# Kernel optimization log

Measured on AMD Instinct MI355X. Metric: run time of the kernel, lower is better.

Reference implementation:

```python
import jax, jax.numpy as jnp
import numpy as np

U = 512   # units
D = 512   # decoder input feature dim
V = 46    # output vocab


def _lstm_cell(x_t, h, c, W, R, b):
    # Keras LSTMCell: gate order i, f, g(cell), o; sigmoid recurrent act, tanh act.
    z = x_t @ W + h @ R + b                      # [B, 4U]
    i, f, g, o = jnp.split(z, 4, axis=-1)
    i = jax.nn.sigmoid(i)
    f = jax.nn.sigmoid(f)
    g = jnp.tanh(g)
    o = jax.nn.sigmoid(o)
    c_new = f * c + i * g
    h_new = o * jnp.tanh(c_new)
    return h_new, c_new


def _lstm_seq(seq, W, R, b):
    # seq: [T, B, D]; zero initial state (Keras default). Returns (all h [T,B,U], last h [B,U]).
    B = seq.shape[1]
    u = R.shape[0]
    h0 = jnp.zeros((B, u), seq.dtype)
    c0 = jnp.zeros((B, u), seq.dtype)
    def step(carry, x_t):
        h, c = carry
        h, c = _lstm_cell(x_t, h, c, W, R, b)
        return (h, c), h
    (hT, _), hs = jax.lax.scan(step, (h0, c0), seq)
    return hs, hT


def setup_inputs() -> dict:
    key = jax.random.key(0)
    ks = jax.random.split(key, 10)
    def p(k, shape, scale=0.05):
        return jax.random.normal(k, shape, dtype=jnp.float32) * scale
    x = jax.random.normal(ks[0], (32, 512, U), dtype=jnp.float32)   # encoder outputs [B, S, U]
    y = jax.random.normal(ks[1], (32, 128, D), dtype=jnp.float32)   # decoder inputs  [B, T, D]
    return {
        "x": x, "y": y,
        "W_a": p(ks[2], (D, 4 * U)), "R_a": p(ks[3], (U, 4 * U)), "b_a": jnp.zeros((4 * U,), jnp.float32),
        "W1": p(ks[4], (U, 4 * U)), "R1": p(ks[5], (U, 4 * U)), "b1": jnp.zeros((4 * U,), jnp.float32),
        "W2": p(ks[6], (U, 4 * U)), "R2": p(ks[7], (U, 4 * U)), "b2": jnp.zeros((4 * U,), jnp.float32),
        "Wd": p(ks[8], (U, V)), "bd": jnp.zeros((V,), jnp.float32),
    }


def reference(x, y, W_a, R_a, b_a, W1, R1, b1, W2, R2, b2, Wd, bd):
    B = y.shape[0]
    yT = jnp.swapaxes(y, 0, 1)                          # [T, B, D]
    h0 = jnp.zeros((B, U), x.dtype)
    c0 = jnp.zeros((B, U), x.dtype)

    # AttentionLSTM: per-step LSTMCell + dot-product attention (Keras Attention,
    # unscaled, keys==values==x) + residual add of the context into both states.
    def step(carry, y_t):
        h, c = carry
        h, c = _lstm_cell(y_t, h, c, W_a, R_a, b_a)     # s = h  [B, U]
        scores = jnp.einsum('bu,bsu->bs', h, x)         # [B, S]
        ctx = jnp.einsum('bs,bsu->bu', jax.nn.softmax(scores, axis=-1), x)  # [B, U]
        return (h + ctx, c + ctx), ctx

    _, ctxs = jax.lax.scan(step, (h0, c0), yT)          # [T, B, U]

    # Stacked LSTMs: first returns full sequence, second returns last hidden state.
    hs1, _ = _lstm_seq(ctxs, W1, R1, b1)                # [T, B, U]
    _, hT = _lstm_seq(hs1, W2, R2, b2)                  # [B, U]

    logits = hT @ Wd + bd                               # [B, V]
    return jax.nn.softmax(logits, axis=-1)
```

## Files before the change

kernel.cpp:

```cpp
#include <hip/hip_runtime.h>
#include <math.h>


#define U_   512
#define S_   512
#define T_   128
#define B_   32
#define G4   2048
#define V_   46
#define NWG  256
#define FSTR 32

#define AT_LD(p)     __hip_atomic_load((p), __ATOMIC_RELAXED, __HIP_MEMORY_SCOPE_AGENT)
#define AT_ST(p, v)  __hip_atomic_store((p), (v), __ATOMIC_RELAXED, __HIP_MEMORY_SCOPE_AGENT)

__device__ __forceinline__ void group_bar(unsigned* gflags, unsigned* ggen,
                                          unsigned seq) {
  __syncthreads();
  const int tid = threadIdx.x;
  const int wgid = blockIdx.x & 31;
  if (wgid == 0) {
    if (tid < 64) {
      if (tid == 0) AT_ST(&gflags[0], seq);
      const int slot = tid & 31;
      while (!__all(AT_LD(&gflags[slot * FSTR]) >= seq))
        __builtin_amdgcn_s_sleep(1);
      if (tid == 0) AT_ST(ggen, seq);
    }
  } else {
    if (tid == 0) {
      AT_ST(&gflags[wgid * FSTR], seq);
      while (AT_LD(ggen) < seq) __builtin_amdgcn_s_sleep(1);
    }
  }
  __syncthreads();
}

__global__ __launch_bounds__(256) void gemm_k512(
    const float* __restrict__ A, const float* __restrict__ W,
    const float* __restrict__ b, float* __restrict__ Z) {
  const int tid = threadIdx.x;
  const int j = blockIdx.x * 1024 + tid * 4;
  const int i0 = blockIdx.y * 8;
  float4 bj = *(const float4*)(b + j);
  float4 acc[8];
#pragma unroll
  for (int r = 0; r < 8; ++r) acc[r] = bj;
  const float* Arow = A + (size_t)i0 * U_;
  for (int k = 0; k < U_; ++k) {
    float4 w = *(const float4*)(W + (size_t)k * G4 + j);
#pragma unroll
    for (int r = 0; r < 8; ++r) {
      float a = Arow[(size_t)r * U_ + k];
      acc[r].x = fmaf(a, w.x, acc[r].x);
      acc[r].y = fmaf(a, w.y, acc[r].y);
      acc[r].z = fmaf(a, w.z, acc[r].z);
      acc[r].w = fmaf(a, w.w, acc[r].w);
    }
  }
#pragma unroll
  for (int r = 0; r < 8; ++r)
    *(float4*)(Z + (size_t)(i0 + r) * G4 + j) = acc[r];
}

__global__ __launch_bounds__(256) void transpose_R(
    const float* __restrict__ R, float* __restrict__ RT) {
  __shared__ float tile[64][65];
  const int c0 = blockIdx.x * 64, k0 = blockIdx.y * 64;
  const int tc = threadIdx.x & 63, tr = threadIdx.x >> 6;
  for (int r = tr; r < 64; r += 4)
    tile[r][tc] = R[(size_t)(k0 + r) * G4 + c0 + tc];
  __syncthreads();
  for (int r = tr; r < 64; r += 4)
    RT[(size_t)(c0 + r) * 512 + k0 + tc] = tile[tc][r];
}

__global__ __launch_bounds__(512) void attn_coop(
    const float* __restrict__ x, const float* __restrict__ ZY,
    const float* __restrict__ RT, float* __restrict__ ctxs,
    float* hbuf, float* hnbuf, float* smax, float* ssumg,
    float* ctxpart, unsigned* flags, unsigned* gen) {
  extern __shared__ float dyn[];
  float* x_s  = dyn;
  float* h_st = dyn + 512 * 65;
  __shared__ float zp[4][64][2];
  __shared__ float hn_s[512];
  __shared__ float p_s[64];

  const int tid = threadIdx.x;
  const int bid = blockIdx.x;
  const int g    = bid >> 5;
  const int wgid = bid & 31;
  const int u0   = wgid * 16;
  const int kh  = tid & 1;
  const int b_l = (tid >> 1) & 3;
  const int col = tid >> 3;
  const int zcol = (col >> 4) * 512 + u0 + (col & 15);
  const int b_att = 4 * g + (wgid >> 3);
  const int sc = wgid & 7;
  unsigned* gflags = flags + g * 32 * FSTR;
  unsigned* ggen   = gen + g * FSTR;

  for (int idx = tid; idx < 64 * 512; idx += 512) {
    int sl = idx >> 9, u = idx & 511;
    x_s[u * 65 + sl] = x[((size_t)b_att * S_ + sc * 64 + sl) * U_ + u];
  }
  float c = 0.f, hn_reg = 0.f;
  unsigned seq = 0;
  __syncthreads();

  for (int t = 0; t < T_; ++t) {
    {
      const float* hb = hbuf + (t & 1) * 16384 + 4 * g * 512;
      for (int i = tid; i < 2048; i += 512)
        h_st[(i >> 9) * 516 + (i & 511)] = AT_LD(&hb[i]);
    }
    __syncthreads();
    {
      const float4* H4 = (const float4*)(h_st + b_l * 516 + kh * 256);
      const float4* R4 = (const float4*)(RT + (size_t)zcol * 512 + kh * 256);
      float acc = 0.f;
#pragma unroll 8
      for (int i = 0; i < 64; ++i) {
        float4 hv = H4[i];
        float4 rv = R4[i];
        acc = fmaf(hv.x, rv.x, acc); acc = fmaf(hv.y, rv.y, acc);
        acc = fmaf(hv.z, rv.z, acc); acc = fmaf(hv.w, rv.w, acc);
      }
      zp[b_l][col][kh] = acc;
    }
    __syncthreads();
    if (tid < 64) {
      const int bb = tid >> 4, uu = tid & 15;
      const int b = 4 * g + bb, u = u0 + uu;
      const float* zy = ZY + ((size_t)b * T_ + t) * G4 + u;
      float zi = zy[0]    + zp[bb][uu][0]      + zp[bb][uu][1];
      float zf = zy[512]  + zp[bb][16 + uu][0] + zp[bb][16 + uu][1];
      float zg = zy[1024] + zp[bb][32 + uu][0] + zp[bb][32 + uu][1];
      float zo = zy[1536] + zp[bb][48 + uu][0] + zp[bb][48 + uu][1];
      float ig = 1.f / (1.f + expf(-zi));
      float fg = 1.f / (1.f + expf(-zf));
      float gg = tanhf(zg);
      float og = 1.f / (1.f + expf(-zo));
      c = fg * c + ig * gg;
      hn_reg = og * tanhf(c);
      AT_ST(&hnbuf[b * 512 + u], hn_reg);
    }
    group_bar(gflags, ggen, ++seq);

    hn_s[tid] = AT_LD(&hnbuf[b_att * 512 + tid]);
    __syncthreads();
    {
      const int wv = tid >> 6, ln = tid & 63;
      for (int si = 0; si < 8; ++si) {
        const int sl = wv * 8 + si;
        float a = 0.f;
#pragma unroll
        for (int uu = ln; uu < 512; uu += 64)
          a = fmaf(hn_s[uu], x_s[uu * 65 + sl], a);
#pragma unroll
        for (int off = 32; off; off >>= 1) a += __shfl_down(a, off);
        if (ln == 0) p_s[sl] = a;
      }
    }
    __syncthreads();
    if (tid < 64) {
      float v = p_s[tid];
      float m = v;
#pragma unroll
      for (int off = 32; off; off >>= 1) m = fmaxf(m, __shfl_down(m, off));
      m = __shfl(m, 0);
      float ex = expf(v - m);
      p_s[tid] = ex;
      float sm = ex;
#pragma unroll
      for (int off = 32; off; off >>= 1) sm += __shfl_down(sm, off);
      if (tid == 0) {
        AT_ST(&smax[b_att * 8 + sc], m);
        AT_ST(&ssumg[b_att * 8 + sc], sm);
      }
    }
    __syncthreads();
    {
      float a = 0.f;
      const float* xr = x_s + tid * 65;
#pragma unroll 8
      for (int s = 0; s < 64; ++s) a = fmaf(p_s[s], xr[s], a);
      AT_ST(&ctxpart[((size_t)b_att * 8 + sc) * 512 + tid], a);
    }
    group_bar(gflags, ggen, ++seq);

    if (tid < 64) {
      const int bb = tid >> 4, uu = tid & 15;
      const int b = 4 * g + bb, u = u0 + uu;
      float lm[8], gm = -INFINITY;
#pragma unroll
      for (int j = 0; j < 8; ++j) {
        lm[j] = AT_LD(&smax[b * 8 + j]);
        gm = fmaxf(gm, lm[j]);
      }
      float stot = 0.f, cs = 0.f;
#pragma unroll
      for (int j = 0; j < 8; ++j) {
        float w = expf(lm[j] - gm);
        stot = fmaf(AT_LD(&ssumg[b * 8 + j]), w, stot);
        cs = fmaf(AT_LD(&ctxpart[((size_t)b * 8 + j) * 512 + u]), w, cs);
      }
      float ctxv = cs / stot;
      c += ctxv;
      float hcar = hn_reg + ctxv;
      AT_ST(&hbuf[((t + 1) & 1) * 16384 + b * 512 + u], hcar);
      ctxs[((size_t)b * T_ + t) * U_ + u] = ctxv;
    }
    group_bar(gflags, ggen, ++seq);
  }
}

__global__ __launch_bounds__(512) void lstm_coop(
    const float* __restrict__ Zin, const float* __restrict__ R,
    float* __restrict__ seq_out, float* __restrict__ last_out,
    float* hbuf, unsigned* flags, unsigned* gen) {
  extern __shared__ float dyn[];
  float* R_s  = dyn;
  float* h_st = dyn + 64 * 516;
  __shared__ float zp[4][64][2];
  const int tid = threadIdx.x;
  const int bid = blockIdx.x;
  const int g    = bid >> 5;
  const int wgid = bid & 31;
  const int u0   = wgid * 16;
  const int kh  = tid & 1;
  const int b_l = (tid >> 1) & 3;
  const int col = tid >> 3;
  unsigned* gflags = flags + g * 32 * FSTR;
  unsigned* ggen   = gen + g * FSTR;

  for (int idx = tid; idx < 64 * 512; idx += 512) {
    int cc = idx & 63, kk = idx >> 6;
    R_s[cc * 516 + kk] = R[(size_t)kk * G4 + (cc >> 4) * 512 + u0 + (cc & 15)];
  }
  float c = 0.f;
  unsigned seq = 0;
  __syncthreads();

  for (int t = 0; t < T_; ++t) {
    {
      const float* hb = hbuf + (t & 1) * 16384 + 4 * g * 512;
      for (int i = tid; i < 2048; i += 512)
        h_st[(i >> 9) * 516 + (i & 511)] = AT_LD(&hb[i]);
    }
    __syncthreads();
    {
      const float4* H4 = (const float4*)(h_st + b_l * 516 + kh * 256);
      const float4* R4 = (const float4*)(R_s + col * 516 + kh * 256);
      float acc = 0.f;
#pragma unroll 8
      for (int i = 0; i < 64; ++i) {
        float4 hv = H4[i];
        float4 rv = R4[i];
        acc = fmaf(hv.x, rv.x, acc); acc = fmaf(hv.y, rv.y, acc);
        acc = fmaf(hv.z, rv.z, acc); acc = fmaf(hv.w, rv.w, acc);
      }
      zp[b_l][col][kh] = acc;
    }
    __syncthreads();
    if (tid < 64) {
      const int bb = tid >> 4, uu = tid & 15;
      const int b = 4 * g + bb, u = u0 + uu;
      const float* zy = Zin + ((size_t)b * T_ + t) * G4 + u;
      float zi = zy[0]    + zp[bb][uu][0]      + zp[bb][uu][1];
      float zf = zy[512]  + zp[bb][16 + uu][0] + zp[bb][16 + uu][1];
      float zg = zy[1024] + zp[bb][32 + uu][0] + zp[bb][32 + uu][1];
      float zo = zy[1536] + zp[bb][48 + uu][0] + zp[bb][48 + uu][1];
      float ig = 1.f / (1.f + expf(-zi));
      float fg = 1.f / (1.f + expf(-zf));
      float gg = tanhf(zg);
      float og = 1.f / (1.f + expf(-zo));
      c = fg * c + ig * gg;
      float hv2 = og * tanhf(c);
      AT_ST(&hbuf[((t + 1) & 1) * 16384 + b * 512 + u], hv2);
      if (seq_out) seq_out[((size_t)b * T_ + t) * U_ + u] = hv2;
      if (last_out && t == T_ - 1) last_out[b * U_ + u] = hv2;
    }
    group_bar(gflags, ggen, ++seq);
  }
}

__global__ __launch_bounds__(64) void final_k(
    const float* __restrict__ hT, const float* __restrict__ Wd,
    const float* __restrict__ bd, float* __restrict__ out) {
  const int b = blockIdx.x;
  const int v = threadIdx.x;
  float acc = (v < V_) ? bd[v] : -INFINITY;
  if (v < V_) {
    for (int k = 0; k < U_; ++k)
      acc = fmaf(hT[(size_t)b * U_ + k], Wd[(size_t)k * V_ + v], acc);
  }
  float m = acc;
#pragma unroll
  for (int off = 32; off; off >>= 1) m = fmaxf(m, __shfl_down(m, off));
  m = __shfl(m, 0);
  float e = (v < V_) ? expf(acc - m) : 0.f;
  float s = e;
#pragma unroll
  for (int off = 32; off; off >>= 1) s += __shfl_down(s, off);
  s = __shfl(s, 0);
  if (v < V_) out[(size_t)b * V_ + v] = e / s;
}

extern "C" void kernel_launch(void* const* d_in, const int* in_sizes, int n_in,
                              void* d_out, int out_size, void* d_ws, size_t ws_size,
                              hipStream_t stream) {
  const float* x   = (const float*)d_in[0];
  const float* y   = (const float*)d_in[1];
  const float* W_a = (const float*)d_in[2];
  const float* R_a = (const float*)d_in[3];
  const float* b_a = (const float*)d_in[4];
  const float* W1  = (const float*)d_in[5];
  const float* R1  = (const float*)d_in[6];
  const float* b1  = (const float*)d_in[7];
  const float* W2  = (const float*)d_in[8];
  const float* R2  = (const float*)d_in[9];
  const float* b2  = (const float*)d_in[10];
  const float* Wd  = (const float*)d_in[11];
  const float* bd  = (const float*)d_in[12];
  float* out = (float*)d_out;

  float* ZBUF = (float*)d_ws;
  float* SEQ  = ZBUF + (size_t)8388608;
  float* RT   = SEQ + (size_t)2097152;
  float* HBUF = RT + (size_t)1048576;
  float* HN   = HBUF + 32768;
  float* SMAX = HN + 16384;
  float* SSUM = SMAX + 256;
  float* CTXP = SSUM + 256;
  float* HT   = CTXP + 131072;
  unsigned* BAR = (unsigned*)(HT + 16384);

  const int GRP = 32 * FSTR;
  const int REGION = 8 * GRP + 8 * FSTR;
  unsigned* FLG_A = BAR;                 unsigned* GEN_A = FLG_A + 8 * GRP;
  unsigned* FLG_1 = BAR + REGION;        unsigned* GEN_1 = FLG_1 + 8 * GRP;
  unsigned* FLG_2 = BAR + 2 * REGION;    unsigned* GEN_2 = FLG_2 + 8 * GRP;

  const int attn_lds = (512 * 65 + 4 * 516) * 4;
  const int lstm_lds = (64 * 516 + 4 * 516) * 4;
  hipFuncSetAttribute((const void*)attn_coop,
                      hipFuncAttributeMaxDynamicSharedMemorySize, attn_lds);
  hipFuncSetAttribute((const void*)lstm_coop,
                      hipFuncAttributeMaxDynamicSharedMemorySize, lstm_lds);

  dim3 ggrid(2, 512);
  hipMemsetAsync(BAR, 0, 3 * REGION * 4, stream);

  gemm_k512<<<ggrid, 256, 0, stream>>>(y, W_a, b_a, ZBUF);
  transpose_R<<<dim3(32, 8), 256, 0, stream>>>(R_a, RT);
  hipMemsetAsync(HBUF, 0, 32768 * 4, stream);
  attn_coop<<<NWG, 512, attn_lds, stream>>>(x, ZBUF, RT, SEQ, HBUF, HN,
                                            SMAX, SSUM, CTXP, FLG_A, GEN_A);
  gemm_k512<<<ggrid, 256, 0, stream>>>(SEQ, W1, b1, ZBUF);
  hipMemsetAsync(HBUF, 0, 32768 * 4, stream);
  lstm_coop<<<NWG, 512, lstm_lds, stream>>>(ZBUF, R1, SEQ, nullptr, HBUF,
                                            FLG_1, GEN_1);
  gemm_k512<<<ggrid, 256, 0, stream>>>(SEQ, W2, b2, ZBUF);
  hipMemsetAsync(HBUF, 0, 32768 * 4, stream);
  lstm_coop<<<NWG, 512, lstm_lds, stream>>>(ZBUF, R2, nullptr, HT, HBUF,
                                            FLG_2, GEN_2);
  final_k<<<B_, 64, 0, stream>>>(HT, Wd, bd, out);
}
```

Baseline: 4.615 ms.

## Replace master-based group barrier with all-poll flags and parallelize context merge

The group barrier changes from a two-hop scheme, where workgroup 0 gathers flags and then publishes a generation word, to one where every workgroup polls all 32 peer flags directly. This removes one round-trip of global-memory latency from each of the three barriers per timestep. The context merge also spreads its 8 partial loads per output across 8 lanes with shuffle reductions instead of serial loads in 64 threads, at the cost of one extra __syncthreads. Direct polling raises contention on the flag lines.

```diff
diff --git a/kernel.cpp b/kernel.cpp
--- a/kernel.cpp
+++ b/kernel.cpp
@@ -14,24 +14,14 @@
 #define AT_LD(p)     __hip_atomic_load((p), __ATOMIC_RELAXED, __HIP_MEMORY_SCOPE_AGENT)
 #define AT_ST(p, v)  __hip_atomic_store((p), (v), __ATOMIC_RELAXED, __HIP_MEMORY_SCOPE_AGENT)
 
-__device__ __forceinline__ void group_bar(unsigned* gflags, unsigned* ggen,
-                                          unsigned seq) {
+__device__ __forceinline__ void group_bar(unsigned* gflags, unsigned seq) {
   __syncthreads();
   const int tid = threadIdx.x;
-  const int wgid = blockIdx.x & 31;
-  if (wgid == 0) {
-    if (tid < 64) {
-      if (tid == 0) AT_ST(&gflags[0], seq);
-      const int slot = tid & 31;
-      while (!__all(AT_LD(&gflags[slot * FSTR]) >= seq))
-        __builtin_amdgcn_s_sleep(1);
-      if (tid == 0) AT_ST(ggen, seq);
-    }
-  } else {
-    if (tid == 0) {
-      AT_ST(&gflags[wgid * FSTR], seq);
-      while (AT_LD(ggen) < seq) __builtin_amdgcn_s_sleep(1);
-    }
+  if (tid < 32) {
+    if (tid == 0)
+      AT_ST(&gflags[(blockIdx.x & 31) * FSTR], seq);
+    while (!__all(AT_LD(&gflags[tid * FSTR]) >= seq))
+      __builtin_amdgcn_s_sleep(1);
   }
   __syncthreads();
 }
@@ -79,13 +69,14 @@
     const float* __restrict__ x, const float* __restrict__ ZY,
     const float* __restrict__ RT, float* __restrict__ ctxs,
     float* hbuf, float* hnbuf, float* smax, float* ssumg,
-    float* ctxpart, unsigned* flags, unsigned* gen) {
+    float* ctxpart, unsigned* flags) {
   extern __shared__ float dyn[];
   float* x_s  = dyn;
   float* h_st = dyn + 512 * 65;
   __shared__ float zp[4][64][2];
   __shared__ float hn_s[512];
   __shared__ float p_s[64];
+  __shared__ float ctx_s[64];
 
   const int tid = threadIdx.x;
   const int bid = blockIdx.x;
@@ -99,7 +90,6 @@
   const int b_att = 4 * g + (wgid >> 3);
   const int sc = wgid & 7;
   unsigned* gflags = flags + g * 32 * FSTR;
-  unsigned* ggen   = gen + g * FSTR;
 
   for (int idx = tid; idx < 64 * 512; idx += 512) {
     int sl = idx >> 9, u = idx & 511;
@@ -146,7 +136,7 @@
       hn_reg = og * tanhf(c);
       AT_ST(&hnbuf[b * 512 + u], hn_reg);
     }
-    group_bar(gflags, ggen, ++seq);
+    group_bar(gflags, ++seq);
 
     hn_s[tid] = AT_LD(&hnbuf[b_att * 512 + tid]);
     __syncthreads();
@@ -188,38 +178,47 @@
       for (int s = 0; s < 64; ++s) a = fmaf(p_s[s], xr[s], a);
       AT_ST(&ctxpart[((size_t)b_att * 8 + sc) * 512 + tid], a);
     }
-    group_bar(gflags, ggen, ++seq);
-
+    group_bar(gflags, ++seq);
+
+    {
+      const int j = tid & 7;
+      const int pair = tid >> 3;
+      const int bb = pair >> 4, uu = pair & 15;
+      const int b = 4 * g + bb, u = u0 + uu;
+      float lm = AT_LD(&smax[b * 8 + j]);
+      float ss = AT_LD(&ssumg[b * 8 + j]);
+      float cp = AT_LD(&ctxpart[((size_t)b * 8 + j) * 512 + u]);
+      float gm = lm;
+#pragma unroll
+      for (int off = 1; off < 8; off <<= 1)
+        gm = fmaxf(gm, __shfl_xor(gm, off));
+      float w = expf(lm - gm);
+      float st = ss * w, cs = cp * w;
+#pragma unroll
+      for (int off = 1; off < 8; off <<= 1) {
+        st += __shfl_xor(st, off);
+        cs += __shfl_xor(cs, off);
+      }
+      if (j == 0) ctx_s[pair] = cs / st;
+    }
+    __syncthreads();
     if (tid < 64) {
       const int bb = tid >> 4, uu = tid & 15;
       const int b = 4 * g + bb, u = u0 + uu;
-      float lm[8], gm = -INFINITY;
-#pragma unroll
-      for (int j = 0; j < 8; ++j) {
-        lm[j] = AT_LD(&smax[b * 8 + j]);
-        gm = fmaxf(gm, lm[j]);
-      }
-      float stot = 0.f, cs = 0.f;
-#pragma unroll
-      for (int j = 0; j < 8; ++j) {
-        float w = expf(lm[j] - gm);
-        stot = fmaf(AT_LD(&ssumg[b * 8 + j]), w, stot);
-        cs = fmaf(AT_LD(&ctxpart[((size_t)b * 8 + j) * 512 + u]), w, cs);
-      }
-      float ctxv = cs / stot;
+      float ctxv = ctx_s[tid];
       c += ctxv;
       float hcar = hn_reg + ctxv;
       AT_ST(&hbuf[((t + 1) & 1) * 16384 + b * 512 + u], hcar);
       ctxs[((size_t)b * T_ + t) * U_ + u] = ctxv;
     }
-    group_bar(gflags, ggen, ++seq);
+    group_bar(gflags, ++seq);
   }
 }
 
 __global__ __launch_bounds__(512) void lstm_coop(
     const float* __restrict__ Zin, const float* __restrict__ R,
     float* __restrict__ seq_out, float* __restrict__ last_out,
-    float* hbuf, unsigned* flags, unsigned* gen) {
+    float* hbuf, unsigned* flags) {
   extern __shared__ float dyn[];
   float* R_s  = dyn;
   float* h_st = dyn + 64 * 516;
@@ -233,7 +232,6 @@
   const int b_l = (tid >> 1) & 3;
   const int col = tid >> 3;
   unsigned* gflags = flags + g * 32 * FSTR;
-  unsigned* ggen   = gen + g * FSTR;
 
   for (int idx = tid; idx < 64 * 512; idx += 512) {
     int cc = idx & 63, kk = idx >> 6;
@@ -282,7 +280,7 @@
       if (seq_out) seq_out[((size_t)b * T_ + t) * U_ + u] = hv2;
       if (last_out && t == T_ - 1) last_out[b * U_ + u] = hv2;
     }
-    group_bar(gflags, ggen, ++seq);
+    group_bar(gflags, ++seq);
   }
 }
 
@@ -337,11 +335,10 @@
   float* HT   = CTXP + 131072;
   unsigned* BAR = (unsigned*)(HT + 16384);
 
-  const int GRP = 32 * FSTR;
-  const int REGION = 8 * GRP + 8 * FSTR;
-  unsigned* FLG_A = BAR;                 unsigned* GEN_A = FLG_A + 8 * GRP;
-  unsigned* FLG_1 = BAR + REGION;        unsigned* GEN_1 = FLG_1 + 8 * GRP;
-  unsigned* FLG_2 = BAR + 2 * REGION;    unsigned* GEN_2 = FLG_2 + 8 * GRP;
+  const int REGION = 8 * 32 * FSTR;
+  unsigned* FLG_A = BAR;
+  unsigned* FLG_1 = BAR + REGION;
+  unsigned* FLG_2 = BAR + 2 * REGION;
 
   const int attn_lds = (512 * 65 + 4 * 516) * 4;
   const int lstm_lds = (64 * 516 + 4 * 516) * 4;
@@ -357,14 +354,14 @@
   transpose_R<<<dim3(32, 8), 256, 0, stream>>>(R_a, RT);
   hipMemsetAsync(HBUF, 0, 32768 * 4, stream);
   attn_coop<<<NWG, 512, attn_lds, stream>>>(x, ZBUF, RT, SEQ, HBUF, HN,
-                                            SMAX, SSUM, CTXP, FLG_A, GEN_A);
+                                            SMAX, SSUM, CTXP, FLG_A);
   gemm_k512<<<ggrid, 256, 0, stream>>>(SEQ, W1, b1, ZBUF);
   hipMemsetAsync(HBUF, 0, 32768 * 4, stream);
   lstm_coop<<<NWG, 512, lstm_lds, stream>>>(ZBUF, R1, SEQ, nullptr, HBUF,
-                                            FLG_1, GEN_1);
+                                            FLG_1);
   gemm_k512<<<ggrid, 256, 0, stream>>>(SEQ, W2, b2, ZBUF);
   hipMemsetAsync(HBUF, 0, 32768 * 4, stream);
   lstm_coop<<<NWG, 512, lstm_lds, stream>>>(ZBUF, R2, nullptr, HT, HBUF,
-                                            FLG_2, GEN_2);
+                                            FLG_2);
   final_k<<<B_, 64, 0, stream>>>(HT, Wd, bd, out);
 }
```

New measurement: 4.389 ms. 4.9% less time.
